# Kernel optimization log

Hardware: AMD Instinct MI355X
Metric: run time of the kernel (lower is better)

## Reference

```python
import jax, jax.numpy as jnp
import numpy as np

N_NODES = 50000
N_PAIRS = 625000
F = 128

def setup_inputs() -> dict:
    key = jax.random.key(0)
    k1, k2, k3, k4, k5 = jax.random.split(key, 5)
    x = jax.random.normal(k1, (N_NODES, F), dtype=jnp.float32)
    alpha_ij = jax.random.normal(k2, (N_PAIRS,), dtype=jnp.float32)
    idx_i = jax.random.randint(k3, (N_PAIRS,), 0, N_NODES, dtype=jnp.int32)
    idx_j = jax.random.randint(k4, (N_PAIRS,), 0, N_NODES, dtype=jnp.int32)
    # Dense(F, use_bias=False) kernel, shape (F_in, F_out)
    W = jax.random.normal(k5, (F, F), dtype=jnp.float32) / np.sqrt(F)
    return {"x": x, "alpha_ij": alpha_ij, "idx_i": idx_i, "idx_j": idx_j, "W": W}

def reference(x, alpha_ij, idx_i, idx_j, W):
    # dense projection on nodes (n,F) @ (F,F) -> (n,F)
    v = jnp.matmul(x, W)
    # gather neighbor values, scale by attention coeff: (n_pairs, F)
    msg = alpha_ij[:, None] * v[idx_j]
    # scatter-sum back to center atoms
    return jax.ops.segment_sum(msg, segment_ids=idx_i, num_segments=x.shape[0])
```

## Files before the change

### kernel.cpp

```cpp
#include <hip/hip_runtime.h>
#include <stdint.h>

#define FDIM 128
#define NB_S 196
#define QC   4096
#define NB_F 784
#define SS   1024
#define PPB  2048
#define CONVB 782

typedef short  s8v   __attribute__((ext_vector_type(8)));
typedef float  f4v   __attribute__((ext_vector_type(4)));
typedef unsigned short u8v __attribute__((ext_vector_type(8)));

__device__ __forceinline__ unsigned short f2bf(float f) {
    union { float f; uint32_t u; } c; c.f = f;
    uint32_t u = c.u;
    return (unsigned short)((u + 0x7fffu + ((u >> 16) & 1u)) >> 16);
}
__device__ __forceinline__ float bflo2f(uint32_t g) {
    union { uint32_t u; float f; } c; c.u = g << 16; return c.f;
}
__device__ __forceinline__ float bfhi2f(uint32_t g) {
    union { uint32_t u; float f; } c; c.u = g & 0xffff0000u; return c.f;
}

__global__ __launch_bounds__(256) void prep(const float* __restrict__ W,
                                            unsigned short* __restrict__ Wt,
                                            int* __restrict__ gcur) {
    int i = blockIdx.x * 256 + threadIdx.x;
    if (i < FDIM * FDIM) {
        int n = i & 127, k = i >> 7;
        Wt[n * FDIM + k] = f2bf(W[k * FDIM + n]);
    }
    if (i < NB_S) gcur[i] = 0;
}

__global__ __launch_bounds__(256) void convert_pass1(
        const float* __restrict__ x,
        unsigned short* __restrict__ xb,
        const int* __restrict__ idx_i,
        const int* __restrict__ idx_j,
        const float* __restrict__ alpha,
        int* __restrict__ gcur,
        unsigned long long* __restrict__ qrec,
        int n_rows, int n_pairs, int PB) {

    if ((int)blockIdx.x < PB) {
        __shared__ int hist[NB_S];
        __shared__ int base_s[NB_S];
        const int t = threadIdx.x;
        const int start = blockIdx.x * PPB;

        if (t < NB_S) hist[t] = 0;
        __syncthreads();

        unsigned long long rec[8];
        int bkt[8];
#pragma unroll
        for (int i = 0; i < 8; ++i) {
            int p = start + t + i * 256;
            bkt[i] = -1;
            if (p < n_pairs) {
                int ii = idx_i[p];
                bkt[i] = ii >> 8;
                rec[i] = (unsigned long long)(uint32_t)(idx_j[p] | ((ii & 255) << 16))
                       | ((unsigned long long)(uint32_t)__float_as_int(alpha[p]) << 32);
                atomicAdd(&hist[bkt[i]], 1);
            }
        }
        __syncthreads();
        if (t < NB_S) {
            int h = hist[t];
            base_s[t] = (h > 0) ? atomicAdd(&gcur[t], h) : 0;
            hist[t] = 0;
        }
        __syncthreads();
#pragma unroll
        for (int i = 0; i < 8; ++i) {
            int b = bkt[i];
            if (b >= 0) {
                int lp  = atomicAdd(&hist[b], 1);
                int pos = base_s[b] + lp;
                if (pos < QC)
                    qrec[(size_t)b * QC + pos] = rec[i];
            }
        }
        return;
    }

    const long long total8 = (long long)n_rows * FDIM / 8;
    long long i8 = (long long)((int)blockIdx.x - PB) * 256 + threadIdx.x;
    const long long stride = (long long)CONVB * 256;
    for (; i8 < total8; i8 += stride) {
        const float* src = x + i8 * 8;
        float4 a = ((const float4*)src)[0];
        float4 b = ((const float4*)src)[1];
        u8v pk;
        pk[0] = f2bf(a.x); pk[1] = f2bf(a.y); pk[2] = f2bf(a.z); pk[3] = f2bf(a.w);
        pk[4] = f2bf(b.x); pk[5] = f2bf(b.y); pk[6] = f2bf(b.z); pk[7] = f2bf(b.w);
        *(u8v*)(xb + i8 * 8) = pk;
    }
}

__global__ __launch_bounds__(512) void agg_gemm(
        const unsigned short* __restrict__ xb,
        const unsigned short* __restrict__ Wt,
        const int* __restrict__ gcur,
        const unsigned long long* __restrict__ qrec,
        float* __restrict__ out,
        int n_nodes) {
    __shared__ unsigned long long sraw[SS];
    __shared__ unsigned long long ssort[SS];
    __shared__ unsigned short sacc[64][FDIM + 8];
    __shared__ int cnt64[64];
    __shared__ int start[65];
    __shared__ int nloc_s;
    const int t    = threadIdx.x;
    const int c    = blockIdx.x;
    const int cb   = c >> 2;
    const int qt   = c & 3;
    const int wv   = t >> 6;
    const int lane = t & 63;

    int nrec = gcur[cb];
    nrec = (nrec > QC) ? QC : nrec;
    const unsigned long long* q = qrec + (size_t)cb * QC;

    if (t < 64) cnt64[t] = 0;
    if (t == 0) nloc_s = 0;
    __syncthreads();

    for (int k = t; k < nrec; k += 512) {
        unsigned long long r = q[k];
        int off8 = (int)((r >> 16) & 255);
        if ((off8 >> 6) == qt) {
            int p = atomicAdd(&nloc_s, 1);
            if (p < SS) sraw[p] = r;
            atomicAdd(&cnt64[off8 & 63], 1);
        }
    }
    __syncthreads();

    if (t < 64) {
        int v0 = cnt64[t];
        int s  = v0;
#pragma unroll
        for (int d = 1; d < 64; d <<= 1) {
            int n = __shfl_up(s, d);
            if (t >= d) s += n;
        }
        start[t]  = s - v0;
        cnt64[t]  = s - v0;
        if (t == 63) start[64] = s;
    }
    __syncthreads();

    int nloc = nloc_s;
    nloc = (nloc > SS) ? SS : nloc;
    for (int k = t; k < nloc; k += 512) {
        unsigned long long r = sraw[k];
        int off = (int)((r >> 16) & 63);
        int pos = atomicAdd(&cnt64[off], 1);
        ssort[pos] = r;
    }
    __syncthreads();

#pragma unroll 1
    for (int i = 0; i < 8; ++i) {
        const int off = wv * 8 + i;
        const int s0 = start[off];
        const int s1 = start[off + 1];

        float ax0 = 0.f, ay0 = 0.f, ax1 = 0.f, ay1 = 0.f;
        int k = s0;
        for (; k + 8 <= s1; k += 8) {
            unsigned long long r[8];
#pragma unroll
            for (int u = 0; u < 8; ++u) r[u] = ssort[k + u];
            uint32_t g[8]; float a[8];
#pragma unroll
            for (int u = 0; u < 8; ++u) {
                int j = (int)(r[u] & 0xffff);
                a[u] = __int_as_float((int)(r[u] >> 32));
                g[u] = *(const uint32_t*)(xb + (size_t)j * FDIM + lane * 2);
            }
#pragma unroll
            for (int u = 0; u < 8; ++u) {
                if (u & 1) { ax1 += a[u] * bflo2f(g[u]); ay1 += a[u] * bfhi2f(g[u]); }
                else       { ax0 += a[u] * bflo2f(g[u]); ay0 += a[u] * bfhi2f(g[u]); }
            }
        }
        if (k + 4 <= s1) {
            unsigned long long r0 = ssort[k],     r1 = ssort[k + 1];
            unsigned long long r2 = ssort[k + 2], r3 = ssort[k + 3];
            int j0 = (int)(r0 & 0xffff), j1 = (int)(r1 & 0xffff);
            int j2 = (int)(r2 & 0xffff), j3 = (int)(r3 & 0xffff);
            float a0 = __int_as_float((int)(r0 >> 32));
            float a1 = __int_as_float((int)(r1 >> 32));
            float a2 = __int_as_float((int)(r2 >> 32));
            float a3 = __int_as_float((int)(r3 >> 32));
            uint32_t g0 = *(const uint32_t*)(xb + (size_t)j0 * FDIM + lane * 2);
            uint32_t g1 = *(const uint32_t*)(xb + (size_t)j1 * FDIM + lane * 2);
            uint32_t g2 = *(const uint32_t*)(xb + (size_t)j2 * FDIM + lane * 2);
            uint32_t g3 = *(const uint32_t*)(xb + (size_t)j3 * FDIM + lane * 2);
            ax0 += a0 * bflo2f(g0) + a2 * bflo2f(g2);
            ay0 += a0 * bfhi2f(g0) + a2 * bfhi2f(g2);
            ax1 += a1 * bflo2f(g1) + a3 * bflo2f(g3);
            ay1 += a1 * bfhi2f(g1) + a3 * bfhi2f(g3);
            k += 4;
        }
        for (; k < s1; ++k) {
            unsigned long long r0 = ssort[k];
            int j0 = (int)(r0 & 0xffff);
            float a0 = __int_as_float((int)(r0 >> 32));
            uint32_t g0 = *(const uint32_t*)(xb + (size_t)j0 * FDIM + lane * 2);
            ax0 += a0 * bflo2f(g0);
            ay0 += a0 * bfhi2f(g0);
        }
        float ax = ax0 + ax1, ay = ay0 + ay1;
        uint32_t packed = (uint32_t)f2bf(ax) | ((uint32_t)f2bf(ay) << 16);
        *(uint32_t*)((char*)&sacc[off][0] + lane * 4) = packed;
    }
    __syncthreads();

    const int rt   = (wv & 3) * 16;
    const int ct   = (wv >> 2) * 64;
    const int lrow = lane & 15;
    const int kq   = (lane >> 4) * 8;

    f4v acc[4];
#pragma unroll
    for (int j = 0; j < 4; ++j) acc[j] = (f4v){0.f, 0.f, 0.f, 0.f};

#pragma unroll
    for (int ks = 0; ks < 4; ++ks) {
        const int k0 = ks * 32 + kq;
        s8v aa = *(const s8v*)(&sacc[rt + lrow][k0]);
        const unsigned short* wb = Wt + (size_t)(ct + lrow) * FDIM + k0;
        s8v b0 = *(const s8v*)(wb);
        s8v b1 = *(const s8v*)(wb + 16 * FDIM);
        s8v b2 = *(const s8v*)(wb + 32 * FDIM);
        s8v b3 = *(const s8v*)(wb + 48 * FDIM);
        acc[0] = __builtin_amdgcn_mfma_f32_16x16x32_bf16(aa, b0, acc[0], 0, 0, 0);
        acc[1] = __builtin_amdgcn_mfma_f32_16x16x32_bf16(aa, b1, acc[1], 0, 0, 0);
        acc[2] = __builtin_amdgcn_mfma_f32_16x16x32_bf16(aa, b2, acc[2], 0, 0, 0);
        acc[3] = __builtin_amdgcn_mfma_f32_16x16x32_bf16(aa, b3, acc[3], 0, 0, 0);
    }

    const int quad = lane >> 4;
#pragma unroll
    for (int j = 0; j < 4; ++j) {
#pragma unroll
        for (int r = 0; r < 4; ++r) {
            int row  = rt + quad * 4 + r;
            int node = c * 64 + row;
            if (node < n_nodes)
                out[(size_t)node * FDIM + ct + j * 16 + lrow] = acc[j][r];
        }
    }
}

extern "C" void kernel_launch(void* const* d_in, const int* in_sizes, int n_in,
                              void* d_out, int out_size, void* d_ws, size_t ws_size,
                              hipStream_t stream) {
    const float* x     = (const float*)d_in[0];
    const float* alpha = (const float*)d_in[1];
    const int*   idx_i = (const int*)d_in[2];
    const int*   idx_j = (const int*)d_in[3];
    const float* W     = (const float*)d_in[4];

    const int n_nodes = in_sizes[0] / FDIM;
    const int n_pairs = in_sizes[1];

    char* ws = (char*)d_ws;
    size_t off = 0;
    auto carve = [&](size_t bytes) {
        char* p = ws + off;
        off += (bytes + 255) & ~(size_t)255;
        return p;
    };
    unsigned short* xb = (unsigned short*)carve((size_t)n_nodes * FDIM * sizeof(unsigned short));
    unsigned short* Wt = (unsigned short*)carve((size_t)FDIM * FDIM * sizeof(unsigned short));
    int*  gcur = (int*)carve((size_t)NB_S * sizeof(int));
    unsigned long long* qrec =
        (unsigned long long*)carve((size_t)NB_S * QC * sizeof(unsigned long long));
    float* out = (float*)d_out;

    prep<<<(FDIM * FDIM + 255) / 256, 256, 0, stream>>>(W, Wt, gcur);

    int PB = (n_pairs + PPB - 1) / PPB;
    convert_pass1<<<PB + CONVB, 256, 0, stream>>>(x, xb, idx_i, idx_j, alpha,
                                                  gcur, qrec, n_nodes, n_pairs, PB);

    agg_gemm<<<NB_F, 512, 0, stream>>>(xb, Wt, gcur, qrec, out, n_nodes);
}
```

Baseline: 136.3 us.

## Replace fixed-capacity bucket queues with histogram-scan compacted bucketing

The single pass that claimed space in fixed 4096-entry per-bucket queues through global atomics is split into three kernels: per-block bucket histograms, a single-block scan that computes exact global offsets, and a placement pass that writes records into a compact array sized to the number of pairs. This removes the QC capacity limit, which could silently drop pairs, and the global atomic contention. In exchange it adds one kernel launch, reads idx_i a second time, and runs a serial scan over blocks. Block sizes also grow to 1024 threads and each placement block handles 8192 pairs.

```diff
diff --git a/kernel.cpp b/kernel.cpp
--- a/kernel.cpp
+++ b/kernel.cpp
@@ -3,10 +3,9 @@
 
 #define FDIM 128
 #define NB_S 196
-#define QC   4096
 #define NB_F 784
 #define SS   1024
-#define PPB  2048
+#define PPB  8192
 #define CONVB 782
 
 typedef short  s8v   __attribute__((ext_vector_type(8)));
@@ -25,73 +24,110 @@
     union { uint32_t u; float f; } c; c.u = g & 0xffff0000u; return c.f;
 }
 
-__global__ __launch_bounds__(256) void prep(const float* __restrict__ W,
-                                            unsigned short* __restrict__ Wt,
-                                            int* __restrict__ gcur) {
-    int i = blockIdx.x * 256 + threadIdx.x;
-    if (i < FDIM * FDIM) {
-        int n = i & 127, k = i >> 7;
-        Wt[n * FDIM + k] = f2bf(W[k * FDIM + n]);
-    }
-    if (i < NB_S) gcur[i] = 0;
-}
-
-__global__ __launch_bounds__(256) void convert_pass1(
+__global__ __launch_bounds__(1024) void hist_prep(
+        const float* __restrict__ W,
+        unsigned short* __restrict__ Wt,
+        const int* __restrict__ idx_i,
+        int* __restrict__ histg,
+        int n_pairs, int PB) {
+    const int t = threadIdx.x;
+    if ((int)blockIdx.x == PB) {
+        for (int i = t; i < FDIM * FDIM; i += 1024) {
+            int n = i & 127, k = i >> 7;
+            Wt[n * FDIM + k] = f2bf(W[k * FDIM + n]);
+        }
+        return;
+    }
+    __shared__ int hist[NB_S];
+    if (t < NB_S) hist[t] = 0;
+    __syncthreads();
+    const int start = blockIdx.x * PPB;
+    int ii[8];
+#pragma unroll
+    for (int i = 0; i < 8; ++i) {
+        int p = start + t + i * 1024;
+        ii[i] = (p < n_pairs) ? idx_i[p] : -1;
+    }
+#pragma unroll
+    for (int i = 0; i < 8; ++i)
+        if (ii[i] >= 0) atomicAdd(&hist[ii[i] >> 8], 1);
+    __syncthreads();
+    if (t < NB_S) histg[blockIdx.x * NB_S + t] = hist[t];
+}
+
+__global__ __launch_bounds__(256) void scan_k(
+        const int* __restrict__ histg,
+        int* __restrict__ baseg,
+        int* __restrict__ Bg,
+        int PB) {
+    __shared__ int tot[256];
+    const int t = threadIdx.x;
+    int running = 0;
+    if (t < NB_S) {
+        for (int blk = 0; blk < PB; ++blk) {
+            int h = histg[blk * NB_S + t];
+            baseg[blk * NB_S + t] = running;
+            running += h;
+        }
+    }
+    tot[t] = (t < NB_S) ? running : 0;
+    __syncthreads();
+    for (int d = 1; d < 256; d <<= 1) {
+        int v = (t >= d) ? tot[t - d] : 0;
+        __syncthreads();
+        tot[t] += v;
+        __syncthreads();
+    }
+    if (t < NB_S) Bg[t] = tot[t] - running;
+    if (t == NB_S - 1) Bg[NB_S] = tot[t];
+}
+
+__global__ __launch_bounds__(1024) void place_convert(
         const float* __restrict__ x,
         unsigned short* __restrict__ xb,
         const int* __restrict__ idx_i,
         const int* __restrict__ idx_j,
         const float* __restrict__ alpha,
-        int* __restrict__ gcur,
+        const int* __restrict__ baseg,
+        const int* __restrict__ Bg,
         unsigned long long* __restrict__ qrec,
         int n_rows, int n_pairs, int PB) {
+    const int t = threadIdx.x;
 
     if ((int)blockIdx.x < PB) {
-        __shared__ int hist[NB_S];
-        __shared__ int base_s[NB_S];
-        const int t = threadIdx.x;
+        __shared__ int cur[NB_S];
+        if (t < NB_S)
+            cur[t] = Bg[t] + baseg[blockIdx.x * NB_S + t];
+        __syncthreads();
         const int start = blockIdx.x * PPB;
-
-        if (t < NB_S) hist[t] = 0;
-        __syncthreads();
-
-        unsigned long long rec[8];
-        int bkt[8];
+        int ii[8], jj[8]; float aa[8];
 #pragma unroll
         for (int i = 0; i < 8; ++i) {
-            int p = start + t + i * 256;
-            bkt[i] = -1;
+            int p = start + t + i * 1024;
+            ii[i] = -1;
             if (p < n_pairs) {
-                int ii = idx_i[p];
-                bkt[i] = ii >> 8;
-                rec[i] = (unsigned long long)(uint32_t)(idx_j[p] | ((ii & 255) << 16))
-                       | ((unsigned long long)(uint32_t)__float_as_int(alpha[p]) << 32);
-                atomicAdd(&hist[bkt[i]], 1);
+                ii[i] = idx_i[p];
+                jj[i] = idx_j[p];
+                aa[i] = alpha[p];
             }
         }
-        __syncthreads();
-        if (t < NB_S) {
-            int h = hist[t];
-            base_s[t] = (h > 0) ? atomicAdd(&gcur[t], h) : 0;
-            hist[t] = 0;
-        }
-        __syncthreads();
 #pragma unroll
         for (int i = 0; i < 8; ++i) {
-            int b = bkt[i];
-            if (b >= 0) {
-                int lp  = atomicAdd(&hist[b], 1);
-                int pos = base_s[b] + lp;
-                if (pos < QC)
-                    qrec[(size_t)b * QC + pos] = rec[i];
+            if (ii[i] >= 0) {
+                int b = ii[i] >> 8;
+                unsigned long long rec =
+                      (unsigned long long)(uint32_t)(jj[i] | ((ii[i] & 255) << 16))
+                    | ((unsigned long long)(uint32_t)__float_as_int(aa[i]) << 32);
+                int pos = atomicAdd(&cur[b], 1);
+                qrec[pos] = rec;
             }
         }
         return;
     }
 
     const long long total8 = (long long)n_rows * FDIM / 8;
-    long long i8 = (long long)((int)blockIdx.x - PB) * 256 + threadIdx.x;
-    const long long stride = (long long)CONVB * 256;
+    long long i8 = (long long)((int)blockIdx.x - PB) * 1024 + t;
+    const long long stride = (long long)CONVB * 1024;
     for (; i8 < total8; i8 += stride) {
         const float* src = x + i8 * 8;
         float4 a = ((const float4*)src)[0];
@@ -106,7 +142,7 @@
 __global__ __launch_bounds__(512) void agg_gemm(
         const unsigned short* __restrict__ xb,
         const unsigned short* __restrict__ Wt,
-        const int* __restrict__ gcur,
+        const int* __restrict__ Bg,
         const unsigned long long* __restrict__ qrec,
         float* __restrict__ out,
         int n_nodes) {
@@ -123,9 +159,9 @@
     const int wv   = t >> 6;
     const int lane = t & 63;
 
-    int nrec = gcur[cb];
-    nrec = (nrec > QC) ? QC : nrec;
-    const unsigned long long* q = qrec + (size_t)cb * QC;
+    const int b0r  = Bg[cb];
+    const int nrec = Bg[cb + 1] - b0r;
+    const unsigned long long* q = qrec + b0r;
 
     if (t < 64) cnt64[t] = 0;
     if (t == 0) nloc_s = 0;
@@ -272,6 +308,7 @@
 
     const int n_nodes = in_sizes[0] / FDIM;
     const int n_pairs = in_sizes[1];
+    const int PB = (n_pairs + PPB - 1) / PPB;
 
     char* ws = (char*)d_ws;
     size_t off = 0;
@@ -282,16 +319,19 @@
     };
     unsigned short* xb = (unsigned short*)carve((size_t)n_nodes * FDIM * sizeof(unsigned short));
     unsigned short* Wt = (unsigned short*)carve((size_t)FDIM * FDIM * sizeof(unsigned short));
-    int*  gcur = (int*)carve((size_t)NB_S * sizeof(int));
+    int* histg = (int*)carve((size_t)PB * NB_S * sizeof(int));
+    int* baseg = (int*)carve((size_t)PB * NB_S * sizeof(int));
+    int* Bg    = (int*)carve((size_t)(NB_S + 1) * sizeof(int));
     unsigned long long* qrec =
-        (unsigned long long*)carve((size_t)NB_S * QC * sizeof(unsigned long long));
+        (unsigned long long*)carve((size_t)n_pairs * sizeof(unsigned long long));
     float* out = (float*)d_out;
 
-    prep<<<(FDIM * FDIM + 255) / 256, 256, 0, stream>>>(W, Wt, gcur);
-
-    int PB = (n_pairs + PPB - 1) / PPB;
-    convert_pass1<<<PB + CONVB, 256, 0, stream>>>(x, xb, idx_i, idx_j, alpha,
-                                                  gcur, qrec, n_nodes, n_pairs, PB);
-
-    agg_gemm<<<NB_F, 512, 0, stream>>>(xb, Wt, gcur, qrec, out, n_nodes);
-}
+    hist_prep<<<PB + 1, 1024, 0, stream>>>(W, Wt, idx_i, histg, n_pairs, PB);
+
+    scan_k<<<1, 256, 0, stream>>>(histg, baseg, Bg, PB);
+
+    place_convert<<<PB + CONVB, 1024, 0, stream>>>(x, xb, idx_i, idx_j, alpha,
+                                                   baseg, Bg, qrec, n_nodes, n_pairs, PB);
+
+    agg_gemm<<<NB_F, 512, 0, stream>>>(xb, Wt, Bg, qrec, out, n_nodes);
+}
```

Measured after the change: 163.6 us. 20.0% more time.
